# Optimization experiments

Hardware: AMD Instinct MI355X
Metric: run time of the kernel (lower is better)

## Reference

```python
import jax, jax.numpy as jnp
import numpy as np
from jax import lax

# YOLOv2-COCO configuration (matches RegionLayer attributes)
NUM = 5            # boxes per cell
CLASSES = 80
COORDS = 4
AL = CLASSES + COORDS + 1   # anchor_len = 85
H = W = 19
BATCH = 128
OBJ_T = 0.5
NMS_T = 0.45
CLS_T = 0.1
ANCHORS = np.array([0.57273, 0.677385, 1.87446, 2.06253, 3.33843,
                    5.47434, 7.88282, 3.52778, 9.77052, 9.16828], np.float32)


def setup_inputs() -> dict:
    key = jax.random.key(0)
    pred = jax.random.uniform(key, (BATCH, NUM * AL, H, W), dtype=jnp.float32)
    anchors = jnp.asarray(ANCHORS)
    return {"pred": pred, "anchors": anchors}


def _decode(pred, anchors):
    """YOLOv2 decode: pred [B, NUM*AL, H, W] -> detections [B, NUM*H*W, 7].
    Columns: [obj, x, y, w, h, cls_id, cls_prob*obj] (image-relative coords)."""
    B, C, h, w = pred.shape
    x = pred.reshape(B, NUM, AL, h, w)
    tx, ty, tw, th, obj = x[:, :, 0], x[:, :, 1], x[:, :, 2], x[:, :, 3], x[:, :, 4]
    cls = x[:, :, 5:]                                   # [B, NUM, CLASSES, h, w]
    ii = jnp.arange(w, dtype=pred.dtype)                # cell x offsets
    jj = jnp.arange(h, dtype=pred.dtype)                # cell y offsets
    bx = (tx + ii[None, None, None, :]) / w
    by = (ty + jj[None, None, :, None]) / h
    aw = anchors[0::2][None, :, None, None]
    ah = anchors[1::2][None, :, None, None]
    bw = jnp.exp(tw) * (aw / w)
    bh = jnp.exp(th) * (ah / h)
    prob = jnp.max(cls, axis=2) * obj                   # max class prob * objectness
    cid = jnp.argmax(cls, axis=2).astype(pred.dtype)
    det = jnp.stack([obj, bx, by, bw, bh, cid, prob], axis=-1)  # [B,NUM,h,w,7]
    return det.reshape(B, NUM * h * w, 7)


def _per_image(det):
    """Greedy NMS (faithful to nms_obj) + result_prob_fliter on one image.
    Returns fixed-shape [N,7]; rejected rows are zeroed (instead of torch's
    variable-length concatenation)."""
    order = jnp.argsort(-det[:, 0])                     # sort by objectness desc
    d = det[order]
    dd = lax.stop_gradient(d)
    valid = dd[:, 0] > OBJ_T                            # strict >, as sign() in torch
    num_obj = jnp.sum(valid.astype(jnp.int32))
    bx, by, bw, bh = dd[:, 1], dd[:, 2], dd[:, 3], dd[:, 4]
    x1, x2 = bx - 0.5 * bw, bx + 0.5 * bw
    y1, y2 = by - 0.5 * bh, by + 0.5 * bh
    area = bw * bh
    N = det.shape[0]
    idxs = jnp.arange(N)

    def body(i, s):
        active = (s[i] > 0.01) & valid[i]
        iw = jnp.maximum(jnp.minimum(x2, x2[i]) - jnp.maximum(x1, x1[i]), 0.0)
        ih = jnp.maximum(jnp.minimum(y2, y2[i]) - jnp.maximum(y1, y1[i]), 0.0)
        inter = iw * ih
        iou = inter / (area + area[i] - inter)
        # torch: mask = max(-sign(iou - t), 0) -> suppress when iou >= t
        supp = active & (idxs > i) & (iou >= NMS_T)
        return jnp.where(supp, 0.0, s)

    s = lax.fori_loop(0, N, body, dd[:, 0])
    # torch loop runs range(num_obj-1): the last surviving-sorted box is never emitted
    keep = valid & (s > 0.01) & (idxs != num_obj - 1)
    # result_prob_fliter: zero class prob below thresh, then filter
    p = d[:, 6] * (lax.stop_gradient(d[:, 6]) > CLS_T).astype(d.dtype)
    final = keep & (lax.stop_gradient(p) > 0.01) & (dd[:, 3] * dd[:, 3] > 0.0004)
    out = jnp.concatenate([d[:, :6], p[:, None]], axis=1)
    return out * final[:, None].astype(out.dtype)


def reference(pred, anchors):
    det = _decode(pred, anchors)            # [B, N, 7]
    return jax.vmap(_per_image)(det)        # [B, N, 7], zeroed rejected rows
```

## Files before the change

kernel.cpp:

```cpp
#include <hip/hip_runtime.h>

#define NUMA 5
#define NCLS 80
#define AL 85
#define HW 361
#define NBOX 1805
#define NBATCH 128
#define NPAD 2048
#define K2T 256
#define MCAP 1024
#define NCHUNK 16
#define NSPLIT 4

#define WS_NUMOBJ_OFF 0
#define WS_ORDER_OFF  512
#define WS_SOBJ_OFF   (512 + NBATCH * NPAD * 2)
#define WS_NEEDED     ((size_t)(WS_SOBJ_OFF + NBATCH * NPAD * 4))
#define WS_SUP_OFF    WS_NEEDED
#define WS_DROW_OFF   (WS_SUP_OFF + (size_t)NBATCH * NCHUNK * MCAP * 8)
#define WS_NEEDED2    (WS_DROW_OFF + (size_t)NBATCH * NCHUNK * 64 * 8)
#define WS_DETW_OFF   WS_NEEDED2
#define WS_NEEDED3    (WS_DETW_OFF + (size_t)NBATCH * NBOX * 7 * 4)

#define MID_CONST (30198987.0 / 67108864.0)

__device__ __forceinline__ unsigned long long bcast64(unsigned long long v, int t) {
    unsigned lo = (unsigned)__builtin_amdgcn_readlane((int)(unsigned)v, t);
    unsigned hi = (unsigned)__builtin_amdgcn_readlane((int)(unsigned)(v >> 32), t);
    return ((unsigned long long)hi << 32) | (unsigned long long)lo;
}

__device__ __forceinline__ bool supp_test(float4 qj, float aj, float4 qi, float ai) {
#pragma clang fp contract(off)
    float iw = fmaxf(fminf(qj.z, qi.z) - fmaxf(qj.x, qi.x), 0.0f);
    float ih = fmaxf(fminf(qj.w, qi.w) - fmaxf(qj.y, qi.y), 0.0f);
    float inter = iw * ih;
    float denom = (aj + ai) - inter;
    float f = fmaf(denom, 0.45f, -inter);
    if (__builtin_expect(fabsf(f) <= denom * 6e-8f, 0)) {
        return fma((double)denom, MID_CONST, -(double)inter) <= 0.0;
    }
    return f < 0.0f;
}

__global__ __launch_bounds__(256) void decode_kernel(
    const float* __restrict__ pred,
    const float* __restrict__ anchors,
    float* __restrict__ det)
{
#pragma clang fp contract(off)
    int id = blockIdx.x * blockDim.x + threadIdx.x;
    if (id >= NBATCH * NBOX) return;
    int b = id / NBOX;
    int r = id - b * NBOX;
    int a = r / HW;
    int s = r - a * HW;
    int ci = s % 19;
    int cj = s / 19;

    const float* base = pred + ((size_t)(b * (NUMA * AL) + a * AL) * HW + s);
    float tx  = base[0 * HW];
    float ty  = base[1 * HW];
    float tw  = base[2 * HW];
    float th  = base[3 * HW];
    float obj = base[4 * HW];

    float cmax = base[5 * HW];
    int karg = 0;
#pragma unroll 4
    for (int k = 1; k < NCLS; ++k) {
        float c = base[(5 + k) * HW];
        if (c > cmax) { cmax = c; karg = k; }
    }

    float bx = (tx + (float)ci) / 19.0f;
    float by = (ty + (float)cj) / 19.0f;
    float aw = anchors[2 * a];
    float ah = anchors[2 * a + 1];
    float bw = expf(tw) * (aw / 19.0f);
    float bh = expf(th) * (ah / 19.0f);
    float prob = cmax * obj;
    float cid  = (float)karg;

    float* o = det + (size_t)(b * NBOX + r) * 7;
    o[0] = obj; o[1] = bx; o[2] = by; o[3] = bw; o[4] = bh; o[5] = cid; o[6] = prob;
}

__global__ __launch_bounds__(1024) void sort_kernel(
    const float* __restrict__ det,
    unsigned short* __restrict__ order_g,
    float* __restrict__ sobj_g,
    int* __restrict__ nobj_g,
    float* __restrict__ detws)
{
    __shared__ unsigned long long keys[NPAD];
    __shared__ int cnt_sh;
    const int b = blockIdx.x;
    const int tid = threadIdx.x;
    const float* detb = det + (size_t)b * NBOX * 7;

    for (int n = tid; n < NPAD; n += 1024) {
        keys[n] = (n < NBOX)
            ? (((unsigned long long)__float_as_uint(detb[n * 7]) << 32)
               | (unsigned long long)(2047 - n))
            : 0ull;
    }
    if (tid == 0) cnt_sh = 0;
    __syncthreads();

    for (unsigned k = 2; k <= NPAD; k <<= 1) {
        for (unsigned j = k >> 1; j > 0; j >>= 1) {
            for (unsigned idx = tid; idx < NPAD; idx += 1024) {
                unsigned ixj = idx ^ j;
                if (ixj > idx) {
                    unsigned long long av = keys[idx], bv = keys[ixj];
                    bool up = ((idx & k) == 0);
                    if (up ? (av < bv) : (av > bv)) { keys[idx] = bv; keys[ixj] = av; }
                }
            }
            __syncthreads();
        }
    }

    int cnt = 0;
    for (int r = tid; r < NBOX; r += 1024) {
        unsigned long long kk = keys[r];
        int idx = 2047 - (int)(unsigned)(kk & 0xffffffffu);
        order_g[b * NPAD + r] = (unsigned short)idx;
        float ob = __uint_as_float((unsigned)(kk >> 32));
        sobj_g[b * NPAD + r] = ob;
        cnt += (ob > 0.5f) ? 1 : 0;
        if (detws) {
            const float* src = detb + idx * 7;
            float* dst = detws + ((size_t)b * NBOX + r) * 7;
#pragma unroll
            for (int q = 0; q < 7; ++q) dst[q] = src[q];
        }
    }
    atomicAdd(&cnt_sh, cnt);
    __syncthreads();
    if (tid == 0) nobj_g[b] = cnt_sh;
}

__global__ __launch_bounds__(1024) void sup_kernel(
    const float* __restrict__ det,
    const unsigned short* __restrict__ order_g,
    const int* __restrict__ nobj_g,
    unsigned long long* __restrict__ sup_g,
    unsigned long long* __restrict__ drow_g,
    const float* __restrict__ detws)
{
#pragma clang fp contract(off)
    __shared__ float4 QS[MCAP];
    __shared__ float  AS[MCAP];
    const int bb = blockIdx.x;
    const int b = bb / NSPLIT;
    const int part = bb - b * NSPLIT;
    const int tid = threadIdx.x;
    const int lane = tid & 63;
    const int wv = tid >> 6;
    const int num_obj = nobj_g[b];
    if (num_obj > MCAP) return;
    const int M = num_obj;
    const int Mc = (M + 63) >> 6;
    const int Atiles = Mc * (Mc + 1) / 2;

    if (detws) {
        const float* src = detws + ((size_t)b * NBOX + tid) * 7;
        float bx = src[1], by = src[2], bw = src[3], bh = src[4];
        QS[tid] = make_float4(bx - 0.5f * bw, by - 0.5f * bh,
                              bx + 0.5f * bw, by + 0.5f * bh);
        AS[tid] = bw * bh;
    } else {
        const float* row = det + (size_t)b * NBOX * 7
                         + (int)order_g[b * NPAD + tid] * 7;
        float bx = row[1], by = row[2], bw = row[3], bh = row[4];
        QS[tid] = make_float4(bx - 0.5f * bw, by - 0.5f * bh,
                              bx + 0.5f * bw, by + 0.5f * bh);
        AS[tid] = bw * bh;
    }
    __syncthreads();

    const int gw = part * 16 + wv;
    const int ks = (gw * Atiles) >> 6;
    const int ke = ((gw + 1) * Atiles) >> 6;
    for (int k = ks; k < ke; ++k) {
        int c2 = 0;
        while ((c2 + 1) * (c2 + 2) / 2 <= k) ++c2;
        int cc = k - c2 * (c2 + 1) / 2;
        int j = c2 * 64 + lane;
        float4 qj = QS[j];
        float  aj = AS[j];
        unsigned long long w = 0ull;
        if (cc == c2) {
            unsigned long long myrow = 0ull;
            for (int t = 0; t < 64; ++t) {
                bool supp = supp_test(qj, aj, QS[cc * 64 + t], AS[cc * 64 + t])
                            && (t < lane);
                unsigned long long bb2 = __ballot(supp);
                w |= supp ? (1ull << t) : 0ull;
                if (lane == t) myrow = bb2;
            }
            drow_g[((size_t)b * NCHUNK + cc) * 64 + lane] = myrow;
        } else {
#pragma unroll 8
            for (int t = 0; t < 64; ++t) {
                bool supp = supp_test(qj, aj, QS[cc * 64 + t], AS[cc * 64 + t]);
                w |= supp ? (1ull << t) : 0ull;
            }
        }
        sup_g[((size_t)b * NCHUNK + cc) * MCAP + j] = w;
    }
}

__global__ __launch_bounds__(256) void scanepi3_kernel(
    float* __restrict__ det,
    const float* __restrict__ detws,
    const float* __restrict__ sobj_g,
    const int* __restrict__ nobj_g,
    const unsigned long long* __restrict__ sup_g,
    const unsigned long long* __restrict__ drow_g)
{
#pragma clang fp contract(off)
    __shared__ unsigned long long SUPL[NCHUNK][MCAP];
    __shared__ unsigned long long DR[NCHUNK][64];
    __shared__ float sobj_l[NPAD];
    const int b = blockIdx.x;
    const int tid = threadIdx.x;
    const int lane = tid & 63;
    float* detb = det + (size_t)b * NBOX * 7;
    const float* dws = detws + (size_t)b * NBOX * 7;
    const int num_obj = nobj_g[b];
    const int M = (num_obj < MCAP) ? num_obj : MCAP;

#pragma unroll
    for (int c = 0; c < 8; ++c)
        sobj_l[tid + c * 256] = sobj_g[b * NPAD + tid + c * 256];

    if (num_obj <= MCAP) {
        const unsigned long long* supb = sup_g + (size_t)b * NCHUNK * MCAP;
#pragma unroll
        for (int i = 0; i < 64; ++i)
            ((unsigned long long*)SUPL)[tid + i * 256] = supb[tid + i * 256];
#pragma unroll
        for (int i = 0; i < 4; ++i)
            ((unsigned long long*)DR)[tid + i * 256] =
                drow_g[(size_t)b * NCHUNK * 64 + tid + i * 256];
        __syncthreads();

        if (tid < 64) {
            unsigned rm = 0u;
            for (int c = 0; c < NCHUNK && c * 64 < M; ++c) {
                int rem_in = M - c * 64;
                unsigned long long cmask =
                    (rem_in >= 64) ? ~0ull : ((1ull << rem_in) - 1ull);
                unsigned long long deadw = __ballot((rm >> c) & 1u);
                unsigned long long rowreg = DR[c][lane];
                unsigned long long rem = cmask & ~deadw;
                const unsigned long long rem0 = rem;
                unsigned long long S = 0ull;
                while (rem) {
                    int t = (int)__builtin_ctzll(rem);
                    S |= (1ull << t);
                    unsigned long long row_t = bcast64(rowreg, t);
                    rem &= ~row_t;
                    rem &= ~(1ull << t);
                }
                unsigned long long deadnew = rem0 & ~S;
                rm |= (unsigned)((deadnew >> lane) & 1ull) << c;
                for (int c2 = c + 1; c2 < NCHUNK && c2 * 64 < M; ++c2) {
                    unsigned long long w2 = SUPL[c][c2 * 64 + lane];
                    rm |= ((w2 & S) != 0ull) ? (1u << c2) : 0u;
                }
            }
#pragma unroll
            for (int c2 = 0; c2 < NCHUNK; ++c2) {
                int j = c2 * 64 + lane;
                if (j < M && ((rm >> c2) & 1u)) sobj_l[j] = 0.0f;
            }
        }
        __syncthreads();
    } else {
        __syncthreads();
        for (int i = 0; i < num_obj; ++i) {
            if (sobj_l[i] > 0.01f) {
                const float* ri = dws + i * 7;
                float bxi = ri[1], byi = ri[2], bwi = ri[3], bhi = ri[4];
                float xi1 = bxi - 0.5f * bwi, xi2 = bxi + 0.5f * bwi;
                float yi1 = byi - 0.5f * bhi, yi2 = byi + 0.5f * bhi;
                float ai = bwi * bhi;
                for (int j = i + 1 + tid; j < num_obj; j += 256) {
                    const float* rj = dws + j * 7;
                    float bxj = rj[1], byj = rj[2], bwj = rj[3], bhj = rj[4];
                    float x1j = bxj - 0.5f * bwj, x2j = bxj + 0.5f * bwj;
                    float y1j = byj - 0.5f * bhj, y2j = byj + 0.5f * bhj;
                    float aj = bwj * bhj;
                    float iw = fmaxf(fminf(x2j, xi2) - fmaxf(x1j, xi1), 0.0f);
                    float ih = fmaxf(fminf(y2j, yi2) - fmaxf(y1j, yi1), 0.0f);
                    float inter = iw * ih;
                    float iou = inter / ((aj + ai) - inter);
                    if (iou >= 0.45f) sobj_l[j] = 0.0f;
                }
            }
            __syncthreads();
        }
    }

#pragma unroll
    for (int c = 0; c < 8; ++c) {
        int r = tid + c * 256;
        if (r < NBOX) {
            const float* src = dws + r * 7;
            float obj = src[0], bx = src[1], by = src[2], bw = src[3];
            float bh = src[4], cid = src[5], prob = src[6];
            float s = sobj_l[r];
            bool keep = (r < num_obj) && (s > 0.01f) && (r != num_obj - 1);
            float p = prob * ((prob > 0.1f) ? 1.0f : 0.0f);
            bool fin = keep && (p > 0.01f) && (bw * bw > 0.0004f);
            float m = fin ? 1.0f : 0.0f;
            float* o = detb + r * 7;
            o[0] = obj * m; o[1] = bx * m; o[2] = by * m; o[3] = bw * m;
            o[4] = bh * m; o[5] = cid * m; o[6] = p * m;
        }
    }
}

__global__ __launch_bounds__(1024, 1) void nms4_kernel(
    const float* __restrict__ det,
    const unsigned short* __restrict__ order_g,
    float* __restrict__ sobj_g,
    const int* __restrict__ nobj_g)
{
#pragma clang fp contract(off)
    __shared__ float4 QS[MCAP];
    __shared__ float  AS[MCAP];
    __shared__ unsigned long long SUP[NCHUNK][MCAP];
    __shared__ unsigned long long DROW[NCHUNK][64];
    const int b = blockIdx.x;
    const int tid = threadIdx.x;
    const int lane = tid & 63;
    const int wv = tid >> 6;
    const float* detb = det + (size_t)b * NBOX * 7;
    const unsigned short* ord = order_g + b * NPAD;
    float* sobj = sobj_g + b * NPAD;
    const int num_obj = nobj_g[b];
    const int M = (num_obj < MCAP) ? num_obj : MCAP;

    if (num_obj <= MCAP) {
        {
            const float* row = detb + (int)ord[tid] * 7;
            float bx = row[1], by = row[2], bw = row[3], bh = row[4];
            QS[tid] = make_float4(bx - 0.5f * bw, by - 0.5f * bh,
                                  bx + 0.5f * bw, by + 0.5f * bh);
            AS[tid] = bw * bh;
        }
        __syncthreads();

        for (int k = wv; k < 136; k += 16) {
            int c2 = 0;
            while ((c2 + 1) * (c2 + 2) / 2 <= k) ++c2;
            int cc = k - c2 * (c2 + 1) / 2;
            if (c2 * 64 < M) {
                int j = c2 * 64 + lane;
                float4 qj = QS[j];
                float  aj = AS[j];
                unsigned long long w = 0ull;
                if (cc == c2) {
                    unsigned long long myrow = 0ull;
                    for (int t = 0; t < 64; ++t) {
                        bool supp = supp_test(qj, aj, QS[cc * 64 + t], AS[cc * 64 + t])
                                    && (t < lane);
                        unsigned long long bb = __ballot(supp);
                        w |= supp ? (1ull << t) : 0ull;
                        if (lane == t) myrow = bb;
                    }
                    DROW[cc][lane] = myrow;
                } else {
#pragma unroll 8
                    for (int t = 0; t < 64; ++t) {
                        bool supp = supp_test(qj, aj, QS[cc * 64 + t], AS[cc * 64 + t]);
                        w |= supp ? (1ull << t) : 0ull;
                    }
                }
                SUP[cc][j] = w;
            }
        }
        __syncthreads();

        if (wv == 0) {
            unsigned rm = 0u;
            for (int c = 0; c < NCHUNK && c * 64 < M; ++c) {
                int rem_in = M - c * 64;
                unsigned long long cmask =
                    (rem_in >= 64) ? ~0ull : ((1ull << rem_in) - 1ull);
                unsigned long long deadw = __ballot((rm >> c) & 1u);
                unsigned long long rowreg = DROW[c][lane];
                unsigned long long rem = cmask & ~deadw;
                const unsigned long long rem0 = rem;
                unsigned long long S = 0ull;
                while (rem) {
                    int t = (int)__builtin_ctzll(rem);
                    S |= (1ull << t);
                    unsigned long long row_t = bcast64(rowreg, t);
                    rem &= ~row_t;
                    rem &= ~(1ull << t);
                }
                unsigned long long deadnew = rem0 & ~S;
                rm |= (unsigned)((deadnew >> lane) & 1ull) << c;
                for (int c2 = c + 1; c2 < NCHUNK && c2 * 64 < M; ++c2) {
                    unsigned long long w2 = SUP[c][c2 * 64 + lane];
                    rm |= ((w2 & S) != 0ull) ? (1u << c2) : 0u;
                }
            }
            for (int c2 = 0; c2 < NCHUNK; ++c2) {
                int j = c2 * 64 + lane;
                if (j < M && ((rm >> c2) & 1u)) sobj[j] = 0.0f;
            }
        }
    } else {
        for (int i = 0; i < num_obj; ++i) {
            if (sobj[i] > 0.01f) {
                const float* ri = detb + (int)ord[i] * 7;
                float bxi = ri[1], byi = ri[2], bwi = ri[3], bhi = ri[4];
                float xi1 = bxi - 0.5f * bwi, xi2 = bxi + 0.5f * bwi;
                float yi1 = byi - 0.5f * bhi, yi2 = byi + 0.5f * bhi;
                float ai = bwi * bhi;
                for (int j = i + 1 + tid; j < num_obj; j += 1024) {
                    const float* rj = detb + (int)ord[j] * 7;
                    float bxj = rj[1], byj = rj[2], bwj = rj[3], bhj = rj[4];
                    float x1j = bxj - 0.5f * bwj, x2j = bxj + 0.5f * bwj;
                    float y1j = byj - 0.5f * bhj, y2j = byj + 0.5f * bhj;
                    float aj = bwj * bhj;
                    float iw = fmaxf(fminf(x2j, xi2) - fmaxf(x1j, xi1), 0.0f);
                    float ih = fmaxf(fminf(y2j, yi2) - fmaxf(y1j, yi1), 0.0f);
                    float inter = iw * ih;
                    float iou = inter / ((aj + ai) - inter);
                    if (iou >= 0.45f) sobj[j] = 0.0f;
                }
            }
            __syncthreads();
        }
    }
}

__global__ __launch_bounds__(256) void epi_kernel(
    float* __restrict__ det,
    const unsigned short* __restrict__ order_g,
    const float* __restrict__ sobj_g,
    const int* __restrict__ nobj_g)
{
#pragma clang fp contract(off)
    const int b = blockIdx.x;
    const int tid = threadIdx.x;
    float* detb = det + (size_t)b * NBOX * 7;
    const unsigned short* ord = order_g + b * NPAD;
    const float* sobj = sobj_g + b * NPAD;
    const int num_obj = nobj_g[b];

    float v0[8], v1[8], v2[8], v3[8], v4[8], v5[8], v6[8], msk[8];
#pragma unroll
    for (int c = 0; c < 8; ++c) {
        int r = tid + c * 256;
        if (r < NBOX) {
            const float* row = detb + (int)ord[r] * 7;
            float obj = row[0], bx = row[1], by = row[2], bw = row[3];
            float bh = row[4], cid = row[5], prob = row[6];
            bool keep = (r < num_obj) && (sobj[r] > 0.01f) && (r != num_obj - 1);
            float p = prob * ((prob > 0.1f) ? 1.0f : 0.0f);
            bool fin = keep && (p > 0.01f) && (bw * bw > 0.0004f);
            v0[c] = obj; v1[c] = bx; v2[c] = by; v3[c] = bw; v4[c] = bh;
            v5[c] = cid; v6[c] = p;
            msk[c] = fin ? 1.0f : 0.0f;
        }
    }
    __syncthreads();
#pragma unroll
    for (int c = 0; c < 8; ++c) {
        int r = tid + c * 256;
        if (r < NBOX) {
            float* o = detb + r * 7;
            o[0] = v0[c] * msk[c];
            o[1] = v1[c] * msk[c];
            o[2] = v2[c] * msk[c];
            o[3] = v3[c] * msk[c];
            o[4] = v4[c] * msk[c];
            o[5] = v5[c] * msk[c];
            o[6] = v6[c] * msk[c];
        }
    }
}

__global__ __launch_bounds__(K2T, 1) void nms_kernel(float* __restrict__ det)
{
#pragma clang fp contract(off)
    __shared__ alignas(16) unsigned long long keys[NPAD];
    __shared__ float s_obj[NBOX];
    __shared__ unsigned short order[NBOX];
    __shared__ int num_obj_sh;

    const int b = blockIdx.x;
    const int tid = threadIdx.x;
    float* detb = det + (size_t)b * NBOX * 7;

    for (int n = tid; n < NPAD; n += K2T) {
        if (n < NBOX) {
            unsigned ob = __float_as_uint(detb[n * 7 + 0]);
            keys[n] = ((unsigned long long)ob << 32) | (unsigned long long)(2047 - n);
        } else keys[n] = 0ull;
    }
    if (tid == 0) num_obj_sh = 0;
    __syncthreads();

    for (unsigned k = 2; k <= NPAD; k <<= 1) {
        for (unsigned j = k >> 1; j > 0; j >>= 1) {
            for (unsigned idx = tid; idx < NPAD; idx += K2T) {
                unsigned ixj = idx ^ j;
                if (ixj > idx) {
                    unsigned long long av = keys[idx], bv = keys[ixj];
                    bool up = ((idx & k) == 0);
                    if (up ? (av < bv) : (av > bv)) { keys[idx] = bv; keys[ixj] = av; }
                }
            }
            __syncthreads();
        }
    }

    int cnt = 0;
    for (int r = tid; r < NBOX; r += K2T) {
        unsigned long long kk = keys[r];
        order[r] = (unsigned short)(2047u - (unsigned)(kk & 0xffffffffu));
        float ob = __uint_as_float((unsigned)(kk >> 32));
        s_obj[r] = ob;
        cnt += (ob > 0.5f) ? 1 : 0;
    }
    atomicAdd(&num_obj_sh, cnt);
    __syncthreads();
    const int num_obj = num_obj_sh;

    for (int i = 0; i < num_obj; ++i) {
        if (s_obj[i] > 0.01f) {
            const float* ri = detb + (int)order[i] * 7;
            float bxi = ri[1], byi = ri[2], bwi = ri[3], bhi = ri[4];
            float xi1 = bxi - 0.5f * bwi, xi2 = bxi + 0.5f * bwi;
            float yi1 = byi - 0.5f * bhi, yi2 = byi + 0.5f * bhi;
            float ai = bwi * bhi;
            for (int j = i + 1 + tid; j < num_obj; j += K2T) {
                const float* rj = detb + (int)order[j] * 7;
                float bxj = rj[1], byj = rj[2], bwj = rj[3], bhj = rj[4];
                float x1j = bxj - 0.5f * bwj, x2j = bxj + 0.5f * bwj;
                float y1j = byj - 0.5f * bhj, y2j = byj + 0.5f * bhj;
                float aj = bwj * bhj;
                float iw = fmaxf(fminf(x2j, xi2) - fmaxf(x1j, xi1), 0.0f);
                float ih = fmaxf(fminf(y2j, yi2) - fmaxf(y1j, yi1), 0.0f);
                float inter = iw * ih;
                float iou = inter / ((aj + ai) - inter);
                if (iou >= 0.45f) s_obj[j] = 0.0f;
            }
        }
        __syncthreads();
    }

    float v0[8], v1[8], v2[8], v3[8], v4[8], v5[8], v6[8], msk[8];
#pragma unroll
    for (int c = 0; c < 8; ++c) {
        int r = tid + c * K2T;
        if (r < NBOX) {
            const float* row = detb + (int)order[r] * 7;
            float obj = row[0], bx = row[1], by = row[2], bw = row[3];
            float bh = row[4], cid = row[5], prob = row[6];
            bool keep = (r < num_obj) && (s_obj[r] > 0.01f) && (r != num_obj - 1);
            float p = prob * ((prob > 0.1f) ? 1.0f : 0.0f);
            bool fin = keep && (p > 0.01f) && (bw * bw > 0.0004f);
            v0[c] = obj; v1[c] = bx; v2[c] = by; v3[c] = bw; v4[c] = bh;
            v5[c] = cid; v6[c] = p;
            msk[c] = fin ? 1.0f : 0.0f;
        }
    }
    __syncthreads();
#pragma unroll
    for (int c = 0; c < 8; ++c) {
        int r = tid + c * K2T;
        if (r < NBOX) {
            float* o = detb + r * 7;
            o[0] = v0[c] * msk[c]; o[1] = v1[c] * msk[c]; o[2] = v2[c] * msk[c];
            o[3] = v3[c] * msk[c]; o[4] = v4[c] * msk[c]; o[5] = v5[c] * msk[c];
            o[6] = v6[c] * msk[c];
        }
    }
}

extern "C" void kernel_launch(void* const* d_in, const int* in_sizes, int n_in,
                              void* d_out, int out_size, void* d_ws, size_t ws_size,
                              hipStream_t stream)
{
    const float* pred    = (const float*)d_in[0];
    const float* anchors = (const float*)d_in[1];
    float* out = (float*)d_out;

    int total = NBATCH * NBOX;
    int blocks = (total + 255) / 256;
    decode_kernel<<<blocks, 256, 0, stream>>>(pred, anchors, out);

    if (ws_size >= WS_NEEDED3) {
        char* ws = (char*)d_ws;
        int*                nobj  = (int*)(ws + WS_NUMOBJ_OFF);
        unsigned short* order     = (unsigned short*)(ws + WS_ORDER_OFF);
        float*              sobj  = (float*)(ws + WS_SOBJ_OFF);
        unsigned long long* sup   = (unsigned long long*)(ws + WS_SUP_OFF);
        unsigned long long* drow  = (unsigned long long*)(ws + WS_DROW_OFF);
        float*              detw  = (float*)(ws + WS_DETW_OFF);
        sort_kernel<<<NBATCH, 1024, 0, stream>>>(out, order, sobj, nobj, detw);
        sup_kernel<<<NBATCH * NSPLIT, 1024, 0, stream>>>(out, order, nobj, sup, drow, detw);
        scanepi3_kernel<<<NBATCH, 256, 0, stream>>>(out, detw, sobj, nobj, sup, drow);
    } else if (ws_size >= WS_NEEDED) {
        char* ws = (char*)d_ws;
        int*            nobj  = (int*)(ws + WS_NUMOBJ_OFF);
        unsigned short* order = (unsigned short*)(ws + WS_ORDER_OFF);
        float*          sobj  = (float*)(ws + WS_SOBJ_OFF);
        sort_kernel<<<NBATCH, 1024, 0, stream>>>(out, order, sobj, nobj, nullptr);
        nms4_kernel<<<NBATCH, 1024, 0, stream>>>(out, order, sobj, nobj);
        epi_kernel<<<NBATCH, 256, 0, stream>>>(out, order, sobj, nobj);
    } else {
        nms_kernel<<<NBATCH, K2T, 0, stream>>>(out);
    }
}
```

Measured before the change: 138.3 us.

## Compact boxes above objectness threshold before sorting, skip sub-threshold work

A new sort kernel first stream-compacts boxes with objectness above the threshold using ballot-based prefix sums. It then bitonic-sorts only up to 1024 keys in a single pass per thread, falling back to the full 2048-key sort when the count exceeds the cap. The epilogue skips loading rows beyond num_obj and writes zeros directly, and the inner suppression loop is fully unrolled. The IoU test now always uses the double-precision fma instead of a float fast path, which may cost throughput on the pairwise stage.

Result: faster. 122.4 us (-11.5%).

```diff
diff --git a/kernel.cpp b/kernel.cpp
--- a/kernel.cpp
+++ b/kernel.cpp
@@ -36,11 +36,7 @@
     float ih = fmaxf(fminf(qj.w, qi.w) - fmaxf(qj.y, qi.y), 0.0f);
     float inter = iw * ih;
     float denom = (aj + ai) - inter;
-    float f = fmaf(denom, 0.45f, -inter);
-    if (__builtin_expect(fabsf(f) <= denom * 6e-8f, 0)) {
-        return fma((double)denom, MID_CONST, -(double)inter) <= 0.0;
-    }
-    return f < 0.0f;
+    return fma((double)denom, MID_CONST, -(double)inter) <= 0.0;
 }
 
 __global__ __launch_bounds__(256) void decode_kernel(
@@ -86,12 +82,125 @@
     o[0] = obj; o[1] = bx; o[2] = by; o[3] = bw; o[4] = bh; o[5] = cid; o[6] = prob;
 }
 
+__global__ __launch_bounds__(1024) void sortc_kernel(
+    const float* __restrict__ det,
+    float* __restrict__ sobj_g,
+    int* __restrict__ nobj_g,
+    float* __restrict__ detws)
+{
+    __shared__ unsigned long long keys[NPAD];
+    __shared__ int c0s[16], c1s[16];
+    __shared__ int ex0s[16], ex1s[16];
+    __shared__ int cnt_sh, totA_sh;
+    const int b = blockIdx.x;
+    const int tid = threadIdx.x;
+    const int lane = tid & 63;
+    const int wv = tid >> 6;
+    const float* detb = det + (size_t)b * NBOX * 7;
+
+    int r0 = tid;
+    int r1 = tid + 1024;
+    float obj0 = detb[r0 * 7];
+    float obj1 = (r1 < NBOX) ? detb[r1 * 7] : -1.0f;
+    bool p0 = obj0 > 0.5f;
+    bool p1 = (r1 < NBOX) && (obj1 > 0.5f);
+    unsigned long long m0 = __ballot(p0);
+    unsigned long long m1 = __ballot(p1);
+    if (lane == 0) { c0s[wv] = __builtin_popcountll(m0); c1s[wv] = __builtin_popcountll(m1); }
+    __syncthreads();
+    if (tid == 0) {
+        int acc = 0;
+        for (int w = 0; w < 16; ++w) { ex0s[w] = acc; acc += c0s[w]; }
+        totA_sh = acc;
+        for (int w = 0; w < 16; ++w) { ex1s[w] = acc; acc += c1s[w]; }
+        cnt_sh = acc;
+    }
+    __syncthreads();
+    const int cnt = cnt_sh;
+    unsigned long long ltm = (1ull << lane) - 1ull;
+
+    if (cnt <= MCAP) {
+        if (p0) {
+            int pos = ex0s[wv] + __builtin_popcountll(m0 & ltm);
+            keys[pos] = ((unsigned long long)__float_as_uint(obj0) << 32)
+                      | (unsigned long long)(2047 - r0);
+        }
+        if (p1) {
+            int pos = ex1s[wv] + __builtin_popcountll(m1 & ltm);
+            keys[pos] = ((unsigned long long)__float_as_uint(obj1) << 32)
+                      | (unsigned long long)(2047 - r1);
+        }
+        if (tid >= cnt) keys[tid] = 0ull;
+        __syncthreads();
+
+        for (unsigned k = 2; k <= 1024; k <<= 1) {
+            for (unsigned j = k >> 1; j > 0; j >>= 1) {
+                unsigned idx = tid;
+                unsigned ixj = idx ^ j;
+                if (ixj > idx) {
+                    unsigned long long av = keys[idx], bv = keys[ixj];
+                    bool up = ((idx & k) == 0);
+                    if (up ? (av < bv) : (av > bv)) { keys[idx] = bv; keys[ixj] = av; }
+                }
+                __syncthreads();
+            }
+        }
+
+        unsigned long long kk = keys[tid];
+        float* dst = detws + ((size_t)b * NBOX + tid) * 7;
+        if (tid < cnt) {
+            int idx = 2047 - (int)(unsigned)(kk & 0xffffffffu);
+            sobj_g[b * NPAD + tid] = __uint_as_float((unsigned)(kk >> 32));
+            const float* src = detb + idx * 7;
+#pragma unroll
+            for (int q = 0; q < 7; ++q) dst[q] = src[q];
+        } else {
+            sobj_g[b * NPAD + tid] = 0.0f;
+#pragma unroll
+            for (int q = 0; q < 7; ++q) dst[q] = 0.0f;
+        }
+        sobj_g[b * NPAD + 1024 + tid] = 0.0f;
+        if (tid == 0) nobj_g[b] = cnt;
+    } else {
+        keys[r0] = ((unsigned long long)__float_as_uint(obj0) << 32)
+                 | (unsigned long long)(2047 - r0);
+        keys[r1] = (r1 < NBOX)
+                 ? (((unsigned long long)__float_as_uint(obj1) << 32)
+                    | (unsigned long long)(2047 - r1))
+                 : 0ull;
+        __syncthreads();
+        for (unsigned k = 2; k <= NPAD; k <<= 1) {
+            for (unsigned j = k >> 1; j > 0; j >>= 1) {
+                for (unsigned idx = tid; idx < NPAD; idx += 1024) {
+                    unsigned ixj = idx ^ j;
+                    if (ixj > idx) {
+                        unsigned long long av = keys[idx], bv = keys[ixj];
+                        bool up = ((idx & k) == 0);
+                        if (up ? (av < bv) : (av > bv)) { keys[idx] = bv; keys[ixj] = av; }
+                    }
+                }
+                __syncthreads();
+            }
+        }
+        for (int r = tid; r < NBOX; r += 1024) {
+            unsigned long long kk = keys[r];
+            int idx = 2047 - (int)(unsigned)(kk & 0xffffffffu);
+            sobj_g[b * NPAD + r] = __uint_as_float((unsigned)(kk >> 32));
+            const float* src = detb + idx * 7;
+            float* dst = detws + ((size_t)b * NBOX + r) * 7;
+#pragma unroll
+            for (int q = 0; q < 7; ++q) dst[q] = src[q];
+        }
+        for (int r = NBOX + tid; r < NPAD; r += 1024) sobj_g[b * NPAD + r] = 0.0f;
+        if (tid == 0) nobj_g[b] = cnt;
+    }
+}
+
 __global__ __launch_bounds__(1024) void sort_kernel(
     const float* __restrict__ det,
     unsigned short* __restrict__ order_g,
     float* __restrict__ sobj_g,
-    int* __restrict__ nobj_g,
-    float* __restrict__ detws)
+    int* __restrict__ nobj_g)
 {
     __shared__ unsigned long long keys[NPAD];
     __shared__ int cnt_sh;
@@ -130,12 +239,6 @@
         float ob = __uint_as_float((unsigned)(kk >> 32));
         sobj_g[b * NPAD + r] = ob;
         cnt += (ob > 0.5f) ? 1 : 0;
-        if (detws) {
-            const float* src = detb + idx * 7;
-            float* dst = detws + ((size_t)b * NBOX + r) * 7;
-#pragma unroll
-            for (int q = 0; q < 7; ++q) dst[q] = src[q];
-        }
     }
     atomicAdd(&cnt_sh, cnt);
     __syncthreads();
@@ -143,8 +246,6 @@
 }
 
 __global__ __launch_bounds__(1024) void sup_kernel(
-    const float* __restrict__ det,
-    const unsigned short* __restrict__ order_g,
     const int* __restrict__ nobj_g,
     unsigned long long* __restrict__ sup_g,
     unsigned long long* __restrict__ drow_g,
@@ -165,16 +266,9 @@
     const int Mc = (M + 63) >> 6;
     const int Atiles = Mc * (Mc + 1) / 2;
 
-    if (detws) {
+    {
         const float* src = detws + ((size_t)b * NBOX + tid) * 7;
         float bx = src[1], by = src[2], bw = src[3], bh = src[4];
-        QS[tid] = make_float4(bx - 0.5f * bw, by - 0.5f * bh,
-                              bx + 0.5f * bw, by + 0.5f * bh);
-        AS[tid] = bw * bh;
-    } else {
-        const float* row = det + (size_t)b * NBOX * 7
-                         + (int)order_g[b * NPAD + tid] * 7;
-        float bx = row[1], by = row[2], bw = row[3], bh = row[4];
         QS[tid] = make_float4(bx - 0.5f * bw, by - 0.5f * bh,
                               bx + 0.5f * bw, by + 0.5f * bh);
         AS[tid] = bw * bh;
@@ -203,7 +297,7 @@
             }
             drow_g[((size_t)b * NCHUNK + cc) * 64 + lane] = myrow;
         } else {
-#pragma unroll 8
+#pragma unroll
             for (int t = 0; t < 64; ++t) {
                 bool supp = supp_test(qj, aj, QS[cc * 64 + t], AS[cc * 64 + t]);
                 w |= supp ? (1ull << t) : 0ull;
@@ -310,17 +404,22 @@
     for (int c = 0; c < 8; ++c) {
         int r = tid + c * 256;
         if (r < NBOX) {
-            const float* src = dws + r * 7;
-            float obj = src[0], bx = src[1], by = src[2], bw = src[3];
-            float bh = src[4], cid = src[5], prob = src[6];
-            float s = sobj_l[r];
-            bool keep = (r < num_obj) && (s > 0.01f) && (r != num_obj - 1);
-            float p = prob * ((prob > 0.1f) ? 1.0f : 0.0f);
-            bool fin = keep && (p > 0.01f) && (bw * bw > 0.0004f);
-            float m = fin ? 1.0f : 0.0f;
             float* o = detb + r * 7;
-            o[0] = obj * m; o[1] = bx * m; o[2] = by * m; o[3] = bw * m;
-            o[4] = bh * m; o[5] = cid * m; o[6] = p * m;
+            if (r < num_obj) {
+                const float* src = dws + r * 7;
+                float obj = src[0], bx = src[1], by = src[2], bw = src[3];
+                float bh = src[4], cid = src[5], prob = src[6];
+                float s = sobj_l[r];
+                bool keep = (s > 0.01f) && (r != num_obj - 1);
+                float p = prob * ((prob > 0.1f) ? 1.0f : 0.0f);
+                bool fin = keep && (p > 0.01f) && (bw * bw > 0.0004f);
+                float m = fin ? 1.0f : 0.0f;
+                o[0] = obj * m; o[1] = bx * m; o[2] = by * m; o[3] = bw * m;
+                o[4] = bh * m; o[5] = cid * m; o[6] = p * m;
+            } else {
+                o[0] = 0.0f; o[1] = 0.0f; o[2] = 0.0f; o[3] = 0.0f;
+                o[4] = 0.0f; o[5] = 0.0f; o[6] = 0.0f;
+            }
         }
     }
 }
@@ -604,20 +703,19 @@
     if (ws_size >= WS_NEEDED3) {
         char* ws = (char*)d_ws;
         int*                nobj  = (int*)(ws + WS_NUMOBJ_OFF);
-        unsigned short* order     = (unsigned short*)(ws + WS_ORDER_OFF);
         float*              sobj  = (float*)(ws + WS_SOBJ_OFF);
         unsigned long long* sup   = (unsigned long long*)(ws + WS_SUP_OFF);
         unsigned long long* drow  = (unsigned long long*)(ws + WS_DROW_OFF);
         float*              detw  = (float*)(ws + WS_DETW_OFF);
-        sort_kernel<<<NBATCH, 1024, 0, stream>>>(out, order, sobj, nobj, detw);
-        sup_kernel<<<NBATCH * NSPLIT, 1024, 0, stream>>>(out, order, nobj, sup, drow, detw);
+        sortc_kernel<<<NBATCH, 1024, 0, stream>>>(out, sobj, nobj, detw);
+        sup_kernel<<<NBATCH * NSPLIT, 1024, 0, stream>>>(nobj, sup, drow, detw);
         scanepi3_kernel<<<NBATCH, 256, 0, stream>>>(out, detw, sobj, nobj, sup, drow);
     } else if (ws_size >= WS_NEEDED) {
         char* ws = (char*)d_ws;
         int*            nobj  = (int*)(ws + WS_NUMOBJ_OFF);
         unsigned short* order = (unsigned short*)(ws + WS_ORDER_OFF);
         float*          sobj  = (float*)(ws + WS_SOBJ_OFF);
-        sort_kernel<<<NBATCH, 1024, 0, stream>>>(out, order, sobj, nobj, nullptr);
+        sort_kernel<<<NBATCH, 1024, 0, stream>>>(out, order, sobj, nobj);
         nms4_kernel<<<NBATCH, 1024, 0, stream>>>(out, order, sobj, nobj);
         epi_kernel<<<NBATCH, 256, 0, stream>>>(out, order, sobj, nobj);
     } else {
```
